# Performance work log

Measured on AMD Instinct MI355X. Metric: run time of the kernel, lower is better.

Reference implementation:

```python
import jax, jax.numpy as jnp
import numpy as np

N = 50000   # nodes
E = 800000  # edges (avg degree 16)
D = 128     # dim_node_features
G = 128     # num_graphs
NP = 25000  # post nodes
NI = 25000  # image nodes
L = 2       # num_gnn_layers
EPS = 1e-5


def setup_inputs() -> dict:
    key = jax.random.key(0)
    ks = jax.random.split(key, 24)
    f = lambda k, shp, s: jax.random.normal(k, shp, jnp.float32) * s
    inp = {
        "x": f(ks[0], (N, D), 1.0),
        "W_gnn": f(ks[1], (L, D, D), D ** -0.5),
        "b_gnn": f(ks[2], (L, D), 0.02),
        "hbn_gamma": 1.0 + f(ks[3], (D,), 0.02),
        "hbn_beta": f(ks[4], (D,), 0.02),
        "gf_w1": f(ks[5], (4 * D, D), (4 * D) ** -0.5),
        "gf_b1": f(ks[6], (D,), 0.02),
        "gf_w2": f(ks[7], (D, D), D ** -0.5),
        "gf_b2": f(ks[8], (D,), 0.02),
        "bn2_gamma": 1.0 + f(ks[9], (D,), 0.02),
        "bn2_beta": f(ks[10], (D,), 0.02),
        "fl_w1": f(ks[11], (D, 64), D ** -0.5),
        "fl_b1": f(ks[12], (64,), 0.02),
        "fl_w2": f(ks[13], (64, 32), 64 ** -0.5),
        "fl_b2": f(ks[14], (32,), 0.02),
        "out_w": f(ks[15], (32, 2), 32 ** -0.5),
        "out_b": f(ks[16], (2,), 0.02),
        "edge_index": jax.random.randint(ks[17], (2, E), 0, N, jnp.int32),
        "post_idx": jax.random.randint(ks[18], (NP,), 0, N, jnp.int32),
        "image_idx": jax.random.randint(ks[19], (NI,), 0, N, jnp.int32),
        "batch_vec": jnp.sort(jax.random.randint(ks[20], (N,), 0, G, jnp.int32)),
    }
    return inp


def _bn(x, gamma, beta):
    # BatchNorm1d, training mode: biased batch statistics
    m = jnp.mean(x, axis=0)
    v = jnp.var(x, axis=0)
    return (x - m) * jax.lax.rsqrt(v + EPS) * gamma + beta


def _mean_pool(feat, seg):
    s = jax.ops.segment_sum(feat, seg, num_segments=G)
    c = jax.ops.segment_sum(jnp.ones(seg.shape[0], feat.dtype), seg, num_segments=G)
    return s / jnp.clip(c, 1.0)[:, None]


def reference(x, W_gnn, b_gnn, hbn_gamma, hbn_beta, gf_w1, gf_b1, gf_w2, gf_b2,
              bn2_gamma, bn2_beta, fl_w1, fl_b1, fl_w2, fl_b2, out_w, out_b,
              edge_index, post_idx, image_idx, batch_vec):
    src, dst = edge_index[0], edge_index[1]
    # GCN symmetric normalization with self loops: deg includes the self loop
    deg = jax.ops.segment_sum(jnp.ones(E, x.dtype), dst, num_segments=N) + 1.0
    dis = deg ** -0.5  # deg^-1/2
    enorm = (dis[src] * dis[dst])[:, None]   # per-edge norm
    snorm = (dis * dis)[:, None]             # self-loop norm
    H = x
    for i in range(L):
        xw = H @ W_gnn[i]                                   # [N, D]
        agg = jax.ops.segment_sum(xw[src] * enorm, dst, num_segments=N)
        H = agg + xw * snorm + b_gnn[i]
        H = jax.nn.leaky_relu(H)
    H = _bn(H, hbn_gamma, hbn_beta)
    pf = _mean_pool(H[post_idx], batch_vec[post_idx])        # [G, D]
    imf = _mean_pool(H[image_idx], batch_vec[image_idx])     # [G, D]
    comb = jnp.concatenate([pf, imf, pf - imf, pf * imf], axis=-1)  # [G, 4D]
    # generate_feature (dropout = identity, eval)
    h = jax.nn.leaky_relu(comb @ gf_w1 + gf_b1) @ gf_w2 + gf_b2
    h = _bn(h, bn2_gamma, bn2_beta)
    # feature_layer (encodeMLP)
    out = jax.nn.leaky_relu(h @ fl_w1 + fl_b1) @ fl_w2 + fl_b2  # [G, 32]
    prob = out @ out_w + out_b                                   # [G, 2]
    return out, prob
```

## Files before the change

kernel.cpp:

```cpp
#include <hip/hip_runtime.h>
#include <hip/hip_bf16.h>
#include <math.h>

#define DF 128
#define PSPLIT 4
#define CHUNK 8192
#define NBK 256
#define LEAKY(x) ((x) > 0.f ? (x) : 0.01f * (x))

typedef __attribute__((ext_vector_type(8))) short short8v;
typedef __attribute__((ext_vector_type(4))) float f32x4;
typedef __attribute__((ext_vector_type(4))) unsigned short u16x4;
typedef __attribute__((ext_vector_type(8))) unsigned short u16x8;

static __device__ __forceinline__ unsigned short f2bf(float f) {
  unsigned u = __float_as_uint(f);
  unsigned r = u + 0x7fffu + ((u >> 16) & 1u);
  return (unsigned short)(r >> 16);
}
static __device__ __forceinline__ float bf2f(unsigned short b) {
  return __uint_as_float(((unsigned)b) << 16);
}

__global__ void fused_pre_k(const int* __restrict__ dst, int* __restrict__ bhist,
                            const int* __restrict__ post_idx, const int* __restrict__ image_idx,
                            const int* __restrict__ batch, int* __restrict__ pcnt,
                            int* __restrict__ icnt,
                            const float* __restrict__ W, unsigned short* __restrict__ Wb,
                            int nE, int NP, int NI, int wTotal, int EB, int PB) {
  int b = blockIdx.x;
  if (b < EB) {
    __shared__ int lh[NBK];
    lh[threadIdx.x] = 0;
    __syncthreads();
    for (int i = b * 256 + threadIdx.x; i < nE; i += EB * 256)
      atomicAdd(&lh[dst[i] >> 8], 1);
    __syncthreads();
    if (lh[threadIdx.x]) atomicAdd(&bhist[threadIdx.x], lh[threadIdx.x]);
  } else if (b < EB + PB) {
    int i = (b - EB) * 256 + threadIdx.x;
    if (i < NP) atomicAdd(&pcnt[batch[post_idx[i]]], 1);
    else if (i < NP + NI) atomicAdd(&icnt[batch[image_idx[i - NP]]], 1);
  } else {
    int i = (b - EB - PB) * 256 + threadIdx.x;
    if (i < wTotal) {
      int layer = i >> 14, o = i & 16383;
      int j = o & 7, l = (o >> 3) & 63, ks = (o >> 9) & 3, ct = (o >> 11) & 3, wc = (o >> 13) & 1;
      int row = ks * 32 + (l >> 4) * 8 + j;
      int col = wc * 64 + ct * 16 + (l & 15);
      Wb[i] = f2bf(W[((size_t)layer << 14) + row * DF + col]);
    }
  }
}

__global__ void __launch_bounds__(1024) scan3_k(
    const int* __restrict__ bhist, int* __restrict__ boff2, int* __restrict__ bcur, int NBUCK,
    const int* __restrict__ pcnt, int* __restrict__ poff, int* __restrict__ pcur,
    const int* __restrict__ icnt, int* __restrict__ ioff, int* __restrict__ icur, int G) {
  const int* in; int* out; int* cur; int n;
  if (blockIdx.x == 0)      { in = bhist; out = boff2; cur = bcur; n = NBUCK; }
  else if (blockIdx.x == 1) { in = pcnt;  out = poff;  cur = pcur; n = G; }
  else                      { in = icnt;  out = ioff;  cur = icur; n = G; }
  __shared__ int sh[1024];
  int v = (threadIdx.x < (unsigned)n) ? in[threadIdx.x] : 0;
  sh[threadIdx.x] = v;
  __syncthreads();
  for (int ofs = 1; ofs < 1024; ofs <<= 1) {
    int t = (threadIdx.x >= (unsigned)ofs) ? sh[threadIdx.x - ofs] : 0;
    __syncthreads();
    sh[threadIdx.x] += t;
    __syncthreads();
  }
  if (threadIdx.x < (unsigned)n) {
    int ex = sh[threadIdx.x] - v;
    out[threadIdx.x] = ex;
    cur[threadIdx.x] = ex;
  }
  if (threadIdx.x == 0) out[n] = sh[1023];
}

__global__ void __launch_bounds__(256) bucket_fill_k(const int* __restrict__ src,
                                                     const int* __restrict__ dst,
                                                     int* __restrict__ bcur,
                                                     int* __restrict__ ebuck, int nE) {
  __shared__ int hist[NBK];
  __shared__ int base[NBK];
  __shared__ int gbase[NBK];
  __shared__ int lpack[CHUNK];
  __shared__ unsigned char lbk[CHUNK];
  int e0 = blockIdx.x * CHUNK;
  int cnt = nE - e0; if (cnt > CHUNK) cnt = CHUNK;
  hist[threadIdx.x] = 0;
  __syncthreads();
  for (int i = threadIdx.x; i < cnt; i += 256)
    atomicAdd(&hist[dst[e0 + i] >> 8], 1);
  __syncthreads();
  int t = threadIdx.x;
  base[t] = hist[t];
  __syncthreads();
  for (int ofs = 1; ofs < NBK; ofs <<= 1) {
    int tv = (t >= ofs) ? base[t - ofs] : 0;
    __syncthreads();
    base[t] += tv;
    __syncthreads();
  }
  int excl = base[t] - hist[t];
  __syncthreads();
  base[t] = excl;
  hist[t] = 0;
  __syncthreads();
  for (int i = threadIdx.x; i < cnt; i += 256) {
    int d = dst[e0 + i], s = src[e0 + i];
    int bk = d >> 8;
    int pos = base[bk] + atomicAdd(&hist[bk], 1);
    lpack[pos] = (s << 8) | (d & 255);
    lbk[pos] = (unsigned char)bk;
  }
  __syncthreads();
  int c = hist[t];
  gbase[t] = c > 0 ? atomicAdd(&bcur[t], c) : 0;
  __syncthreads();
  for (int i = threadIdx.x; i < cnt; i += 256) {
    int bk = lbk[i];
    ebuck[gbase[bk] + (i - base[bk])] = lpack[i];
  }
}

__global__ void __launch_bounds__(256) csr_build_k(const int* __restrict__ boff2,
                                                   const int* __restrict__ ebuck,
                                                   int* __restrict__ rowoff,
                                                   float* __restrict__ dis,
                                                   int2* __restrict__ epack,
                                                   int N, int NBUCK) {
  int b = blockIdx.x;
  int beg = boff2[b], end = boff2[b + 1];
  int node0 = b << 8;
  __shared__ int hist[NBK];
  __shared__ int lbase[NBK];
  int t = threadIdx.x;
  hist[t] = 0;
  __syncthreads();
  for (int i = beg + t; i < end; i += 256)
    atomicAdd(&hist[ebuck[i] & 255], 1);
  __syncthreads();
  int v = hist[t];
  lbase[t] = v;
  __syncthreads();
  for (int ofs = 1; ofs < NBK; ofs <<= 1) {
    int tv = (t >= ofs) ? lbase[t - ofs] : 0;
    __syncthreads();
    lbase[t] += tv;
    __syncthreads();
  }
  int excl = lbase[t] - v;
  __syncthreads();
  lbase[t] = excl;
  hist[t] = 0;
  int node = node0 + t;
  if (node < N) {
    rowoff[node] = beg + excl;
    dis[node] = 1.0f / sqrtf((float)v + 1.0f);
  }
  if (b == NBUCK - 1 && t == 0) rowoff[N] = end;
  __syncthreads();
  for (int i = beg + t; i < end; i += 256) {
    int e = ebuck[i];
    int loc = e & 255;
    int pos = beg + lbase[loc] + atomicAdd(&hist[loc], 1);
    int2 w; w.x = e >> 8; w.y = node0 + loc;
    epack[pos] = w;
  }
}

__global__ void enorm_k(int2* __restrict__ epack, const float* __restrict__ dis, int E) {
  int i = blockIdx.x * 256 + threadIdx.x;
  if (i < E) {
    int2 w = epack[i];
    epack[i].y = __float_as_int(dis[w.x] * dis[w.y]);
  }
}

__global__ void pool_fill_k(const int* __restrict__ post_idx, const int* __restrict__ image_idx,
                            const int* __restrict__ batch, int* __restrict__ pcur,
                            int* __restrict__ icur, int* __restrict__ plist,
                            int* __restrict__ ilist, int NP, int NI) {
  int i = blockIdx.x * 256 + threadIdx.x;
  if (i < NP) {
    int nd = post_idx[i];
    int p = atomicAdd(&pcur[batch[nd]], 1);
    plist[p] = nd;
  } else if (i < NP + NI) {
    int nd = image_idx[i - NP];
    int p = atomicAdd(&icur[batch[nd]], 1);
    ilist[p] = nd;
  }
}

template<bool BF16A>
__global__ void __launch_bounds__(256) gemm_mfma_k(const float* __restrict__ A,
                                                   const unsigned short* __restrict__ Ab,
                                                   const unsigned short* __restrict__ Wb,
                                                   unsigned short* __restrict__ xwb, int n) {
  const int w = threadIdx.x >> 6, l = threadIdx.x & 63;
  const int wr = w & 1, wc = w >> 1;
  const int r0 = blockIdx.x * 32 + wr * 16;
  const int row = r0 + (l & 15);
  const int kg = l >> 4;
  short8v bf[4][4];
  const unsigned short* wp = Wb + (size_t)wc * 8192 + (size_t)l * 8;
#pragma unroll
  for (int ct = 0; ct < 4; ++ct)
#pragma unroll
    for (int ks = 0; ks < 4; ++ks)
      bf[ct][ks] = *(const short8v*)(wp + ((ct * 4 + ks) << 9));
  const bool rok = row < n;
  short8v af[4];
  if constexpr (BF16A) {
    const unsigned short* ap = Ab + (size_t)row * DF + kg * 8;
#pragma unroll
    for (int ks = 0; ks < 4; ++ks)
      af[ks] = rok ? *(const short8v*)(ap + ks * 32) : (short8v)0;
  } else {
    const float* ap = A + (size_t)row * DF + kg * 8;
#pragma unroll
    for (int ks = 0; ks < 4; ++ks) {
      if (rok) {
        float4 lo = *(const float4*)(ap + ks * 32);
        float4 hi = *(const float4*)(ap + ks * 32 + 4);
        short8v t;
        t[0] = (short)f2bf(lo.x); t[1] = (short)f2bf(lo.y);
        t[2] = (short)f2bf(lo.z); t[3] = (short)f2bf(lo.w);
        t[4] = (short)f2bf(hi.x); t[5] = (short)f2bf(hi.y);
        t[6] = (short)f2bf(hi.z); t[7] = (short)f2bf(hi.w);
        af[ks] = t;
      } else af[ks] = (short8v)0;
    }
  }
  f32x4 acc[4];
#pragma unroll
  for (int ct = 0; ct < 4; ++ct) acc[ct] = (f32x4)(0.f);
#pragma unroll
  for (int ks = 0; ks < 4; ++ks)
#pragma unroll
    for (int ct = 0; ct < 4; ++ct)
      acc[ct] = __builtin_amdgcn_mfma_f32_16x16x32_bf16(af[ks], bf[ct][ks], acc[ct], 0, 0, 0);
#pragma unroll
  for (int ct = 0; ct < 4; ++ct) {
    int c = wc * 64 + ct * 16 + (l & 15);
#pragma unroll
    for (int rg = 0; rg < 4; ++rg) {
      int r = r0 + kg * 4 + rg;
      if (r < n) xwb[(size_t)r * DF + c] = f2bf(acc[ct][rg]);
    }
  }
}

__global__ void gather_k(const unsigned short* __restrict__ xwb, const int* __restrict__ rowoff,
                         const int2* __restrict__ epack, const float* __restrict__ dis,
                         const float* __restrict__ b, unsigned short* __restrict__ Hb, int n) {
  int gid = blockIdx.x * 256 + threadIdx.x;
  int node = gid >> 5;
  if (node >= n) return;
  int part = gid & 15;
  int team = (gid >> 4) & 1;
  int beg = rowoff[node], end = rowoff[node + 1];
  float acc[8];
#pragma unroll
  for (int j = 0; j < 8; ++j) acc[j] = 0.f;
  int p = beg + team;
  for (; p + 6 < end; p += 8) {
    int2 q0 = epack[p], q1 = epack[p + 2], q2 = epack[p + 4], q3 = epack[p + 6];
    float e0 = __int_as_float(q0.y), e1 = __int_as_float(q1.y);
    float e2 = __int_as_float(q2.y), e3 = __int_as_float(q3.y);
    u16x8 v0 = *(const u16x8*)(xwb + (size_t)q0.x * DF + part * 8);
    u16x8 v1 = *(const u16x8*)(xwb + (size_t)q1.x * DF + part * 8);
    u16x8 v2 = *(const u16x8*)(xwb + (size_t)q2.x * DF + part * 8);
    u16x8 v3 = *(const u16x8*)(xwb + (size_t)q3.x * DF + part * 8);
#pragma unroll
    for (int j = 0; j < 8; ++j) {
      acc[j] = fmaf(bf2f(v0[j]), e0, acc[j]);
      acc[j] = fmaf(bf2f(v1[j]), e1, acc[j]);
      acc[j] = fmaf(bf2f(v2[j]), e2, acc[j]);
      acc[j] = fmaf(bf2f(v3[j]), e3, acc[j]);
    }
  }
  for (; p < end; p += 2) {
    int2 q = epack[p];
    float e = __int_as_float(q.y);
    u16x8 v = *(const u16x8*)(xwb + (size_t)q.x * DF + part * 8);
#pragma unroll
    for (int j = 0; j < 8; ++j) acc[j] = fmaf(bf2f(v[j]), e, acc[j]);
  }
#pragma unroll
  for (int j = 0; j < 8; ++j) acc[j] += __shfl_down(acc[j], 16, 32);
  if (team == 0) {
    float dd = dis[node], sn = dd * dd;
    u16x8 xv = *(const u16x8*)(xwb + (size_t)node * DF + part * 8);
    const float* bp = b + part * 8;
    u16x8 o;
#pragma unroll
    for (int j = 0; j < 8; ++j) {
      float r = fmaf(bf2f(xv[j]), sn, acc[j]) + bp[j];
      r = LEAKY(r);
      o[j] = f2bf(r);
    }
    *(u16x8*)(Hb + (size_t)node * DF + part * 8) = o;
  }
}

__global__ void post_k(const unsigned short* __restrict__ Hb,
                       const int* __restrict__ goff_p, const int* __restrict__ mlist_p,
                       const int* __restrict__ goff_i, const int* __restrict__ mlist_i,
                       float* __restrict__ psum, float* __restrict__ isum,
                       float* __restrict__ bns, int n, int PGB, int SB) {
  int b = blockIdx.x;
  if (b < 2 * PGB) {
    int which = b >= PGB;
    int bb = which ? b - PGB : b;
    const int* goff  = which ? goff_i  : goff_p;
    const int* mlist = which ? mlist_i : mlist_p;
    float* out       = which ? isum    : psum;
    int g = bb / PSPLIT, sub = bb % PSPLIT;
    int part = threadIdx.x & 31, slot = threadIdx.x >> 5;
    int beg = goff[g], end = goff[g + 1];
    float4 acc = make_float4(0.f, 0.f, 0.f, 0.f);
    for (int j = beg + sub * 8 + slot; j < end; j += PSPLIT * 8) {
      u16x4 v = *(const u16x4*)(Hb + (size_t)mlist[j] * DF + part * 4);
      acc.x += bf2f(v[0]); acc.y += bf2f(v[1]); acc.z += bf2f(v[2]); acc.w += bf2f(v[3]);
    }
    __shared__ float4 sh[256];
    sh[threadIdx.x] = acc;
    __syncthreads();
    for (int ofs = 128; ofs >= 32; ofs >>= 1) {
      if (threadIdx.x < (unsigned)ofs) {
        float4 o = sh[threadIdx.x + ofs];
        float4 a = sh[threadIdx.x];
        a.x += o.x; a.y += o.y; a.z += o.z; a.w += o.w;
        sh[threadIdx.x] = a;
      }
      __syncthreads();
    }
    if (threadIdx.x < 32) {
      float4 a = sh[threadIdx.x];
      float* o = out + (size_t)g * DF + part * 4;
      atomicAdd(o + 0, a.x);
      atomicAdd(o + 1, a.y);
      atomicAdd(o + 2, a.z);
      atomicAdd(o + 3, a.w);
    }
  } else {
    int sb = b - 2 * PGB;
    int c = threadIdx.x & (DF - 1);
    int half = threadIdx.x >> 7;
    float s = 0.f, q = 0.f;
    for (int r = sb * 2 + half; r < n; r += SB * 2) {
      float v = bf2f(Hb[(size_t)r * DF + c]);
      s += v; q += v * v;
    }
    __shared__ float ls[256], lq[256];
    ls[threadIdx.x] = s; lq[threadIdx.x] = q;
    __syncthreads();
    if (half == 0) {
      atomicAdd(&bns[c], ls[c] + ls[c + DF]);
      atomicAdd(&bns[DF + c], lq[c] + lq[c + DF]);
    }
  }
}

__global__ void __launch_bounds__(512) head1_k(const float* __restrict__ psum,
                        const int* __restrict__ pcnt,
                        const float* __restrict__ isum, const int* __restrict__ icnt,
                        const float* __restrict__ bns, const float* __restrict__ hbn_gamma,
                        const float* __restrict__ hbn_beta, int nN,
                        const float* __restrict__ gf_w1, const float* __restrict__ gf_b1,
                        const float* __restrict__ gf_w2, const float* __restrict__ gf_b2,
                        float* __restrict__ hbuf) {
  int g = blockIdx.x;
  int j = threadIdx.x & 127, kq = threadIdx.x >> 7;
  __shared__ float comb[4 * DF];
  __shared__ float part[512];
  __shared__ float t1[DF];
  if (kq == 0) {
    float m = bns[j] / (float)nN;
    float var = bns[DF + j] / (float)nN - m * m;
    if (var < 0.f) var = 0.f;
    float sc = hbn_gamma[j] / sqrtf(var + 1e-5f);
    float sh = hbn_beta[j] - m * sc;
    int pc = pcnt[g], ic = icnt[g];
    float pf = pc > 0 ? (psum[(size_t)g * DF + j] / (float)pc) * sc + sh : 0.f;
    float im = ic > 0 ? (isum[(size_t)g * DF + j] / (float)ic) * sc + sh : 0.f;
    comb[j] = pf;
    comb[DF + j] = im;
    comb[2 * DF + j] = pf - im;
    comb[3 * DF + j] = pf * im;
  }
  __syncthreads();
  float acc = 0.f;
  const float* w1 = gf_w1 + (size_t)kq * 128 * DF + j;
#pragma unroll 8
  for (int kk = 0; kk < 128; ++kk)
    acc = fmaf(comb[kq * 128 + kk], w1[(size_t)kk * DF], acc);
  part[threadIdx.x] = acc;
  __syncthreads();
  if (kq == 0)
    t1[j] = LEAKY(gf_b1[j] + part[j] + part[128 + j] + part[256 + j] + part[384 + j]);
  __syncthreads();
  acc = 0.f;
  const float* w2 = gf_w2 + (size_t)kq * 32 * DF + j;
#pragma unroll 8
  for (int kk = 0; kk < 32; ++kk)
    acc = fmaf(t1[kq * 32 + kk], w2[(size_t)kk * DF], acc);
  part[threadIdx.x] = acc;
  __syncthreads();
  if (kq == 0)
    hbuf[(size_t)g * DF + j] = gf_b2[j] + part[j] + part[128 + j] + part[256 + j] + part[384 + j];
}

__global__ void __launch_bounds__(1024) bn2_k(const float* __restrict__ hbuf,
                      const float* __restrict__ gamma, const float* __restrict__ beta,
                      float* __restrict__ ss2, int G) {
  int c = threadIdx.x & 127, slot = threadIdx.x >> 7;
  float s = 0.f, q = 0.f;
  for (int r = slot; r < G; r += 8) {
    float v = hbuf[(size_t)r * DF + c];
    s += v; q += v * v;
  }
  __shared__ float ls[1024], lq[1024];
  ls[threadIdx.x] = s; lq[threadIdx.x] = q;
  __syncthreads();
  for (int ofs = 512; ofs >= 128; ofs >>= 1) {
    if (threadIdx.x < (unsigned)ofs) {
      ls[threadIdx.x] += ls[threadIdx.x + ofs];
      lq[threadIdx.x] += lq[threadIdx.x + ofs];
    }
    __syncthreads();
  }
  if (threadIdx.x < 128) {
    float m = ls[c] / (float)G;
    float var = lq[c] / (float)G - m * m;
    if (var < 0.f) var = 0.f;
    float sc = gamma[c] / sqrtf(var + 1e-5f);
    ss2[c] = sc;
    ss2[DF + c] = beta[c] - m * sc;
  }
}

__global__ void __launch_bounds__(512) head2_k(const float* __restrict__ hbuf,
                        const float* __restrict__ ss2,
                        const float* __restrict__ fl_w1, const float* __restrict__ fl_b1,
                        const float* __restrict__ fl_w2, const float* __restrict__ fl_b2,
                        const float* __restrict__ out_w, const float* __restrict__ out_b,
                        float* __restrict__ d_out, int G) {
  int g = blockIdx.x, t = threadIdx.x;
  __shared__ float hb[DF], part[512], t1[64], ov[32];
  if (t < DF) hb[t] = hbuf[(size_t)g * DF + t] * ss2[t] + ss2[DF + t];
  __syncthreads();
  {
    int j = t & 63, kq = t >> 6;
    float acc = 0.f;
    const float* w = fl_w1 + (size_t)kq * 16 * 64 + j;
#pragma unroll
    for (int kk = 0; kk < 16; ++kk)
      acc = fmaf(hb[kq * 16 + kk], w[(size_t)kk * 64], acc);
    part[t] = acc;
  }
  __syncthreads();
  if (t < 64) {
    float s = fl_b1[t];
#pragma unroll
    for (int i = 0; i < 8; ++i) s += part[i * 64 + t];
    t1[t] = LEAKY(s);
  }
  __syncthreads();
  {
    int j = t & 31, kq = t >> 5;
    float acc = 0.f;
    const float* w = fl_w2 + (size_t)kq * 4 * 32 + j;
#pragma unroll
    for (int kk = 0; kk < 4; ++kk)
      acc = fmaf(t1[kq * 4 + kk], w[(size_t)kk * 32], acc);
    part[t] = acc;
  }
  __syncthreads();
  if (t < 32) {
    float s = fl_b2[t];
#pragma unroll
    for (int i = 0; i < 16; ++i) s += part[i * 32 + t];
    d_out[(size_t)g * 32 + t] = s;
    ov[t] = s;
  }
  __syncthreads();
  if (t < 64) {
    int j = t & 1, kq = t >> 1;
    part[t] = ov[kq] * out_w[(size_t)kq * 2 + j];
  }
  __syncthreads();
  if (t < 2) {
    float s = out_b[t];
#pragma unroll
    for (int i = 0; i < 32; ++i) s += part[i * 2 + t];
    d_out[(size_t)G * 32 + (size_t)g * 2 + t] = s;
  }
}

extern "C" void kernel_launch(void* const* d_in, const int* in_sizes, int n_in,
                              void* d_out, int out_size, void* d_ws, size_t ws_size,
                              hipStream_t stream) {
  const float* x         = (const float*)d_in[0];
  const float* W_gnn     = (const float*)d_in[1];
  const float* b_gnn     = (const float*)d_in[2];
  const float* hbn_gamma = (const float*)d_in[3];
  const float* hbn_beta  = (const float*)d_in[4];
  const float* gf_w1     = (const float*)d_in[5];
  const float* gf_b1     = (const float*)d_in[6];
  const float* gf_w2     = (const float*)d_in[7];
  const float* gf_b2     = (const float*)d_in[8];
  const float* bn2_gamma = (const float*)d_in[9];
  const float* bn2_beta  = (const float*)d_in[10];
  const float* fl_w1     = (const float*)d_in[11];
  const float* fl_b1     = (const float*)d_in[12];
  const float* fl_w2     = (const float*)d_in[13];
  const float* fl_b2     = (const float*)d_in[14];
  const float* out_w     = (const float*)d_in[15];
  const float* out_b     = (const float*)d_in[16];
  const int* edge_index  = (const int*)d_in[17];
  const int* post_idx    = (const int*)d_in[18];
  const int* image_idx   = (const int*)d_in[19];
  const int* batch_vec   = (const int*)d_in[20];

  const int N  = in_sizes[20];
  const int E  = in_sizes[17] / 2;
  const int NP = in_sizes[18];
  const int NI = in_sizes[19];
  const int G  = out_size / 34;
  const int L  = in_sizes[1] / (DF * DF);
  const int* src  = edge_index;
  const int* dstp = edge_index + E;
  const int NBUCK = (N + 255) >> 8;
  const int EB = 256;
  const int PB = (NP + NI + 255) / 256;
  const int WT = L * DF * DF;
  const int WB = (WT + 255) / 256;
  const int PGB = G * PSPLIT;
  const int SB = 256;

  char* ws = (char*)d_ws;
  size_t off = 0;
  auto alloc = [&](size_t b) { size_t o = off; off += (b + 255) & ~(size_t)255; return o; };
  size_t zero_beg = off;
  int*   bhist  = (int*)(ws + alloc((size_t)NBK * 4));
  float* bns    = (float*)(ws + alloc(256 * 4));
  float* psum   = (float*)(ws + alloc((size_t)G * DF * 4));
  float* isum   = (float*)(ws + alloc((size_t)G * DF * 4));
  int*   pcnt   = (int*)(ws + alloc((size_t)G * 4));
  int*   icnt   = (int*)(ws + alloc((size_t)G * 4));
  size_t zero_bytes = off - zero_beg;
  float* dis    = (float*)(ws + alloc((size_t)N * 4));
  int*   rowoff = (int*)(ws + alloc((size_t)(N + 1) * 4));
  int2*  epack  = (int2*)(ws + alloc((size_t)E * 8));
  int*   ebuck  = (int*)(ws + alloc((size_t)E * 4));
  int*   boff2  = (int*)(ws + alloc((size_t)(NBK + 1) * 4));
  int*   bcur   = (int*)(ws + alloc((size_t)NBK * 4));
  unsigned short* Wb  = (unsigned short*)(ws + alloc((size_t)WT * 2));
  unsigned short* xwb = (unsigned short*)(ws + alloc((size_t)N * DF * 2));
  unsigned short* Hb  = (unsigned short*)(ws + alloc((size_t)N * DF * 2));
  int*   poff   = (int*)(ws + alloc((size_t)(G + 1) * 4));
  int*   ioff   = (int*)(ws + alloc((size_t)(G + 1) * 4));
  int*   pcur   = (int*)(ws + alloc((size_t)G * 4));
  int*   icur   = (int*)(ws + alloc((size_t)G * 4));
  int*   plist  = (int*)(ws + alloc((size_t)NP * 4));
  int*   ilist  = (int*)(ws + alloc((size_t)NI * 4));
  float* hbuf   = (float*)(ws + alloc((size_t)G * DF * 4));
  float* ss2    = (float*)(ws + alloc(256 * 4));

  hipMemsetAsync(ws + zero_beg, 0, zero_bytes, stream);

  fused_pre_k<<<EB + PB + WB, 256, 0, stream>>>(dstp, bhist, post_idx, image_idx,
                                                batch_vec, pcnt, icnt, W_gnn, Wb,
                                                E, NP, NI, WT, EB, PB);
  scan3_k<<<3, 1024, 0, stream>>>(bhist, boff2, bcur, NBUCK,
                                  pcnt, poff, pcur, icnt, ioff, icur, G);
  bucket_fill_k<<<(E + CHUNK - 1) / CHUNK, 256, 0, stream>>>(src, dstp, bcur, ebuck, E);
  csr_build_k<<<NBUCK, 256, 0, stream>>>(boff2, ebuck, rowoff, dis, epack, N, NBUCK);
  enorm_k<<<(E + 255) / 256, 256, 0, stream>>>(epack, dis, E);
  pool_fill_k<<<(NP + NI + 255) / 256, 256, 0, stream>>>(post_idx, image_idx, batch_vec,
                                                         pcur, icur, plist, ilist, NP, NI);

  for (int l = 0; l < L; ++l) {
    if (l == 0)
      gemm_mfma_k<false><<<(N + 31) / 32, 256, 0, stream>>>(x, nullptr,
          Wb + (size_t)l * DF * DF, xwb, N);
    else
      gemm_mfma_k<true><<<(N + 31) / 32, 256, 0, stream>>>(nullptr, Hb,
          Wb + (size_t)l * DF * DF, xwb, N);
    gather_k<<<(N * 32 + 255) / 256, 256, 0, stream>>>(xwb, rowoff, epack, dis,
                                                       b_gnn + (size_t)l * DF, Hb, N);
  }

  post_k<<<2 * PGB + SB, 256, 0, stream>>>(Hb, poff, plist, ioff, ilist,
                                           psum, isum, bns, N, PGB, SB);

  head1_k<<<G, 512, 0, stream>>>(psum, pcnt, isum, icnt, bns, hbn_gamma, hbn_beta, N,
                                 gf_w1, gf_b1, gf_w2, gf_b2, hbuf);
  bn2_k<<<1, 1024, 0, stream>>>(hbuf, bn2_gamma, bn2_beta, ss2, G);
  head2_k<<<G, 512, 0, stream>>>(hbuf, ss2, fl_w1, fl_b1, fl_w2, fl_b2, out_w, out_b,
                                 (float*)d_out, G);
}
```

Before: 237.0 us.

## Use fixed-capacity edge buckets and fuse preprocessing kernels to cut launches

```diff
diff --git a/kernel.cpp b/kernel.cpp
--- a/kernel.cpp
+++ b/kernel.cpp
@@ -6,6 +6,7 @@
 #define PSPLIT 4
 #define CHUNK 8192
 #define NBK 256
+#define CAP 6144
 #define LEAKY(x) ((x) > 0.f ? (x) : 0.01f * (x))
 
 typedef __attribute__((ext_vector_type(8))) short short8v;
@@ -22,27 +23,18 @@
   return __uint_as_float(((unsigned)b) << 16);
 }
 
-__global__ void fused_pre_k(const int* __restrict__ dst, int* __restrict__ bhist,
-                            const int* __restrict__ post_idx, const int* __restrict__ image_idx,
-                            const int* __restrict__ batch, int* __restrict__ pcnt,
-                            int* __restrict__ icnt,
-                            const float* __restrict__ W, unsigned short* __restrict__ Wb,
-                            int nE, int NP, int NI, int wTotal, int EB, int PB) {
+__global__ void fusedA_k(const int* __restrict__ post_idx, const int* __restrict__ image_idx,
+                         const int* __restrict__ batch, int* __restrict__ pcnt,
+                         int* __restrict__ icnt,
+                         const float* __restrict__ W, unsigned short* __restrict__ Wb,
+                         int NP, int NI, int wTotal, int PB) {
   int b = blockIdx.x;
-  if (b < EB) {
-    __shared__ int lh[NBK];
-    lh[threadIdx.x] = 0;
-    __syncthreads();
-    for (int i = b * 256 + threadIdx.x; i < nE; i += EB * 256)
-      atomicAdd(&lh[dst[i] >> 8], 1);
-    __syncthreads();
-    if (lh[threadIdx.x]) atomicAdd(&bhist[threadIdx.x], lh[threadIdx.x]);
-  } else if (b < EB + PB) {
-    int i = (b - EB) * 256 + threadIdx.x;
+  if (b < PB) {
+    int i = b * 256 + threadIdx.x;
     if (i < NP) atomicAdd(&pcnt[batch[post_idx[i]]], 1);
     else if (i < NP + NI) atomicAdd(&icnt[batch[image_idx[i - NP]]], 1);
   } else {
-    int i = (b - EB - PB) * 256 + threadIdx.x;
+    int i = (b - PB) * 256 + threadIdx.x;
     if (i < wTotal) {
       int layer = i >> 14, o = i & 16383;
       int j = o & 7, l = (o >> 3) & 63, ks = (o >> 9) & 3, ct = (o >> 11) & 3, wc = (o >> 13) & 1;
@@ -51,32 +43,6 @@
       Wb[i] = f2bf(W[((size_t)layer << 14) + row * DF + col]);
     }
   }
-}
-
-__global__ void __launch_bounds__(1024) scan3_k(
-    const int* __restrict__ bhist, int* __restrict__ boff2, int* __restrict__ bcur, int NBUCK,
-    const int* __restrict__ pcnt, int* __restrict__ poff, int* __restrict__ pcur,
-    const int* __restrict__ icnt, int* __restrict__ ioff, int* __restrict__ icur, int G) {
-  const int* in; int* out; int* cur; int n;
-  if (blockIdx.x == 0)      { in = bhist; out = boff2; cur = bcur; n = NBUCK; }
-  else if (blockIdx.x == 1) { in = pcnt;  out = poff;  cur = pcur; n = G; }
-  else                      { in = icnt;  out = ioff;  cur = icur; n = G; }
-  __shared__ int sh[1024];
-  int v = (threadIdx.x < (unsigned)n) ? in[threadIdx.x] : 0;
-  sh[threadIdx.x] = v;
-  __syncthreads();
-  for (int ofs = 1; ofs < 1024; ofs <<= 1) {
-    int t = (threadIdx.x >= (unsigned)ofs) ? sh[threadIdx.x - ofs] : 0;
-    __syncthreads();
-    sh[threadIdx.x] += t;
-    __syncthreads();
-  }
-  if (threadIdx.x < (unsigned)n) {
-    int ex = sh[threadIdx.x] - v;
-    out[threadIdx.x] = ex;
-    cur[threadIdx.x] = ex;
-  }
-  if (threadIdx.x == 0) out[n] = sh[1023];
 }
 
 __global__ void __launch_bounds__(256) bucket_fill_k(const int* __restrict__ src,
@@ -118,7 +84,7 @@
   }
   __syncthreads();
   int c = hist[t];
-  gbase[t] = c > 0 ? atomicAdd(&bcur[t], c) : 0;
+  gbase[t] = c > 0 ? (t * CAP + atomicAdd(&bcur[t], c)) : 0;
   __syncthreads();
   for (int i = threadIdx.x; i < cnt; i += 256) {
     int bk = lbk[i];
@@ -126,22 +92,51 @@
   }
 }
 
-__global__ void __launch_bounds__(256) csr_build_k(const int* __restrict__ boff2,
+__global__ void __launch_bounds__(1024) scan3_k(
+    const int* __restrict__ bcur, int* __restrict__ boff2, int NBUCK,
+    const int* __restrict__ pcnt, int* __restrict__ poff, int* __restrict__ pcur,
+    const int* __restrict__ icnt, int* __restrict__ ioff, int* __restrict__ icur, int G) {
+  const int* in; int* out; int* cur; int n;
+  if (blockIdx.x == 0)      { in = bcur; out = boff2; cur = nullptr; n = NBUCK; }
+  else if (blockIdx.x == 1) { in = pcnt; out = poff;  cur = pcur;    n = G; }
+  else                      { in = icnt; out = ioff;  cur = icur;    n = G; }
+  __shared__ int sh[1024];
+  int v = (threadIdx.x < (unsigned)n) ? in[threadIdx.x] : 0;
+  sh[threadIdx.x] = v;
+  __syncthreads();
+  for (int ofs = 1; ofs < 1024; ofs <<= 1) {
+    int t = (threadIdx.x >= (unsigned)ofs) ? sh[threadIdx.x - ofs] : 0;
+    __syncthreads();
+    sh[threadIdx.x] += t;
+    __syncthreads();
+  }
+  if (threadIdx.x < (unsigned)n) {
+    int ex = sh[threadIdx.x] - v;
+    out[threadIdx.x] = ex;
+    if (cur) cur[threadIdx.x] = ex;
+  }
+  if (threadIdx.x == 0) out[n] = sh[1023];
+}
+
+__global__ void __launch_bounds__(256) csr_build_k(const int* __restrict__ bcnt,
+                                                   const int* __restrict__ boff2,
                                                    const int* __restrict__ ebuck,
                                                    int* __restrict__ rowoff,
                                                    float* __restrict__ dis,
                                                    int2* __restrict__ epack,
                                                    int N, int NBUCK) {
   int b = blockIdx.x;
-  int beg = boff2[b], end = boff2[b + 1];
+  int cnt = bcnt[b];
+  int ob = boff2[b];
+  const int* ebk = ebuck + (size_t)b * CAP;
   int node0 = b << 8;
   __shared__ int hist[NBK];
   __shared__ int lbase[NBK];
   int t = threadIdx.x;
   hist[t] = 0;
   __syncthreads();
-  for (int i = beg + t; i < end; i += 256)
-    atomicAdd(&hist[ebuck[i] & 255], 1);
+  for (int i = t; i < cnt; i += 256)
+    atomicAdd(&hist[ebk[i] & 255], 1);
   __syncthreads();
   int v = hist[t];
   lbase[t] = v;
@@ -158,52 +153,29 @@
   hist[t] = 0;
   int node = node0 + t;
   if (node < N) {
-    rowoff[node] = beg + excl;
+    rowoff[node] = ob + excl;
     dis[node] = 1.0f / sqrtf((float)v + 1.0f);
   }
-  if (b == NBUCK - 1 && t == 0) rowoff[N] = end;
-  __syncthreads();
-  for (int i = beg + t; i < end; i += 256) {
-    int e = ebuck[i];
+  if (b == NBUCK - 1 && t == 0) rowoff[N] = ob + cnt;
+  __syncthreads();
+  for (int i = t; i < cnt; i += 256) {
+    int e = ebk[i];
     int loc = e & 255;
-    int pos = beg + lbase[loc] + atomicAdd(&hist[loc], 1);
+    int pos = ob + lbase[loc] + atomicAdd(&hist[loc], 1);
     int2 w; w.x = e >> 8; w.y = node0 + loc;
     epack[pos] = w;
   }
 }
 
-__global__ void enorm_k(int2* __restrict__ epack, const float* __restrict__ dis, int E) {
-  int i = blockIdx.x * 256 + threadIdx.x;
-  if (i < E) {
-    int2 w = epack[i];
-    epack[i].y = __float_as_int(dis[w.x] * dis[w.y]);
-  }
-}
-
-__global__ void pool_fill_k(const int* __restrict__ post_idx, const int* __restrict__ image_idx,
-                            const int* __restrict__ batch, int* __restrict__ pcur,
-                            int* __restrict__ icur, int* __restrict__ plist,
-                            int* __restrict__ ilist, int NP, int NI) {
-  int i = blockIdx.x * 256 + threadIdx.x;
-  if (i < NP) {
-    int nd = post_idx[i];
-    int p = atomicAdd(&pcur[batch[nd]], 1);
-    plist[p] = nd;
-  } else if (i < NP + NI) {
-    int nd = image_idx[i - NP];
-    int p = atomicAdd(&icur[batch[nd]], 1);
-    ilist[p] = nd;
-  }
-}
-
 template<bool BF16A>
-__global__ void __launch_bounds__(256) gemm_mfma_k(const float* __restrict__ A,
-                                                   const unsigned short* __restrict__ Ab,
-                                                   const unsigned short* __restrict__ Wb,
-                                                   unsigned short* __restrict__ xwb, int n) {
-  const int w = threadIdx.x >> 6, l = threadIdx.x & 63;
+static __device__ __forceinline__ void gemm_body(int bid, int tid,
+                                                 const float* __restrict__ A,
+                                                 const unsigned short* __restrict__ Ab,
+                                                 const unsigned short* __restrict__ Wb,
+                                                 unsigned short* __restrict__ xwb, int n) {
+  const int w = tid >> 6, l = tid & 63;
   const int wr = w & 1, wc = w >> 1;
-  const int r0 = blockIdx.x * 32 + wr * 16;
+  const int r0 = bid * 32 + wr * 16;
   const int row = r0 + (l & 15);
   const int kg = l >> 4;
   short8v bf[4][4];
@@ -255,6 +227,43 @@
   }
 }
 
+__global__ void __launch_bounds__(256) gemm_mfma_k(const unsigned short* __restrict__ Ab,
+                                                   const unsigned short* __restrict__ Wb,
+                                                   unsigned short* __restrict__ xwb, int n) {
+  gemm_body<true>(blockIdx.x, threadIdx.x, nullptr, Ab, Wb, xwb, n);
+}
+
+__global__ void __launch_bounds__(256) fusedB_k(const float* __restrict__ x,
+                        const unsigned short* __restrict__ Wb, unsigned short* __restrict__ xwb,
+                        int2* __restrict__ epack, const float* __restrict__ dis, int E,
+                        const int* __restrict__ post_idx, const int* __restrict__ image_idx,
+                        const int* __restrict__ batch, int* __restrict__ pcur,
+                        int* __restrict__ icur, int* __restrict__ plist,
+                        int* __restrict__ ilist, int NP, int NI,
+                        int n, int GB, int EN) {
+  int b = blockIdx.x;
+  if (b < GB) {
+    gemm_body<false>(b, threadIdx.x, x, nullptr, Wb, xwb, n);
+  } else if (b < GB + EN) {
+    int i = (b - GB) * 256 + threadIdx.x;
+    if (i < E) {
+      int2 w = epack[i];
+      epack[i].y = __float_as_int(dis[w.x] * dis[w.y]);
+    }
+  } else {
+    int i = (b - GB - EN) * 256 + threadIdx.x;
+    if (i < NP) {
+      int nd = post_idx[i];
+      int p = atomicAdd(&pcur[batch[nd]], 1);
+      plist[p] = nd;
+    } else if (i < NP + NI) {
+      int nd = image_idx[i - NP];
+      int p = atomicAdd(&icur[batch[nd]], 1);
+      ilist[p] = nd;
+    }
+  }
+}
+
 __global__ void gather_k(const unsigned short* __restrict__ xwb, const int* __restrict__ rowoff,
                          const int2* __restrict__ epack, const float* __restrict__ dis,
                          const float* __restrict__ b, unsigned short* __restrict__ Hb, int n) {
@@ -268,6 +277,20 @@
 #pragma unroll
   for (int j = 0; j < 8; ++j) acc[j] = 0.f;
   int p = beg + team;
+  for (; p + 14 < end; p += 16) {
+    int2 q[8];
+#pragma unroll
+    for (int u = 0; u < 8; ++u) q[u] = epack[p + 2 * u];
+    u16x8 v[8];
+#pragma unroll
+    for (int u = 0; u < 8; ++u) v[u] = *(const u16x8*)(xwb + (size_t)q[u].x * DF + part * 8);
+#pragma unroll
+    for (int u = 0; u < 8; ++u) {
+      float e = __int_as_float(q[u].y);
+#pragma unroll
+      for (int j = 0; j < 8; ++j) acc[j] = fmaf(bf2f(v[u][j]), e, acc[j]);
+    }
+  }
   for (; p + 6 < end; p += 8) {
     int2 q0 = epack[p], q1 = epack[p + 2], q2 = epack[p + 4], q3 = epack[p + 6];
     float e0 = __int_as_float(q0.y), e1 = __int_as_float(q1.y);
@@ -537,10 +560,11 @@
   const int* src  = edge_index;
   const int* dstp = edge_index + E;
   const int NBUCK = (N + 255) >> 8;
-  const int EB = 256;
   const int PB = (NP + NI + 255) / 256;
   const int WT = L * DF * DF;
   const int WB = (WT + 255) / 256;
+  const int GB = (N + 31) / 32;
+  const int EN = (E + 255) / 256;
   const int PGB = G * PSPLIT;
   const int SB = 256;
 
@@ -548,7 +572,7 @@
   size_t off = 0;
   auto alloc = [&](size_t b) { size_t o = off; off += (b + 255) & ~(size_t)255; return o; };
   size_t zero_beg = off;
-  int*   bhist  = (int*)(ws + alloc((size_t)NBK * 4));
+  int*   bcur   = (int*)(ws + alloc((size_t)NBK * 4));
   float* bns    = (float*)(ws + alloc(256 * 4));
   float* psum   = (float*)(ws + alloc((size_t)G * DF * 4));
   float* isum   = (float*)(ws + alloc((size_t)G * DF * 4));
@@ -558,9 +582,8 @@
   float* dis    = (float*)(ws + alloc((size_t)N * 4));
   int*   rowoff = (int*)(ws + alloc((size_t)(N + 1) * 4));
   int2*  epack  = (int2*)(ws + alloc((size_t)E * 8));
-  int*   ebuck  = (int*)(ws + alloc((size_t)E * 4));
+  int*   ebuck  = (int*)(ws + alloc((size_t)NBUCK * CAP * 4));
   int*   boff2  = (int*)(ws + alloc((size_t)(NBK + 1) * 4));
-  int*   bcur   = (int*)(ws + alloc((size_t)NBK * 4));
   unsigned short* Wb  = (unsigned short*)(ws + alloc((size_t)WT * 2));
   unsigned short* xwb = (unsigned short*)(ws + alloc((size_t)N * DF * 2));
   unsigned short* Hb  = (unsigned short*)(ws + alloc((size_t)N * DF * 2));
@@ -575,24 +598,18 @@
 
   hipMemsetAsync(ws + zero_beg, 0, zero_bytes, stream);
 
-  fused_pre_k<<<EB + PB + WB, 256, 0, stream>>>(dstp, bhist, post_idx, image_idx,
-                                                batch_vec, pcnt, icnt, W_gnn, Wb,
-                                                E, NP, NI, WT, EB, PB);
-  scan3_k<<<3, 1024, 0, stream>>>(bhist, boff2, bcur, NBUCK,
-                                  pcnt, poff, pcur, icnt, ioff, icur, G);
   bucket_fill_k<<<(E + CHUNK - 1) / CHUNK, 256, 0, stream>>>(src, dstp, bcur, ebuck, E);
-  csr_build_k<<<NBUCK, 256, 0, stream>>>(boff2, ebuck, rowoff, dis, epack, N, NBUCK);
-  enorm_k<<<(E + 255) / 256, 256, 0, stream>>>(epack, dis, E);
-  pool_fill_k<<<(NP + NI + 255) / 256, 256, 0, stream>>>(post_idx, image_idx, batch_vec,
-                                                         pcur, icur, plist, ilist, NP, NI);
-
-  for (int l = 0; l < L; ++l) {
-    if (l == 0)
-      gemm_mfma_k<false><<<(N + 31) / 32, 256, 0, stream>>>(x, nullptr,
-          Wb + (size_t)l * DF * DF, xwb, N);
-    else
-      gemm_mfma_k<true><<<(N + 31) / 32, 256, 0, stream>>>(nullptr, Hb,
-          Wb + (size_t)l * DF * DF, xwb, N);
+  fusedA_k<<<PB + WB, 256, 0, stream>>>(post_idx, image_idx, batch_vec, pcnt, icnt,
+                                        W_gnn, Wb, NP, NI, WT, PB);
+  scan3_k<<<3, 1024, 0, stream>>>(bcur, boff2, NBUCK, pcnt, poff, pcur, icnt, ioff, icur, G);
+  csr_build_k<<<NBUCK, 256, 0, stream>>>(bcur, boff2, ebuck, rowoff, dis, epack, N, NBUCK);
+  fusedB_k<<<GB + EN + PB, 256, 0, stream>>>(x, Wb, xwb, epack, dis, E,
+                                             post_idx, image_idx, batch_vec,
+                                             pcur, icur, plist, ilist, NP, NI, N, GB, EN);
+  gather_k<<<(N * 32 + 255) / 256, 256, 0, stream>>>(xwb, rowoff, epack, dis,
+                                                     b_gnn, Hb, N);
+  for (int l = 1; l < L; ++l) {
+    gemm_mfma_k<<<GB, 256, 0, stream>>>(Hb, Wb + (size_t)l * DF * DF, xwb, N);
     gather_k<<<(N * 32 + 255) / 256, 256, 0, stream>>>(xwb, rowoff, epack, dis,
                                                        b_gnn + (size_t)l * DF, Hb, N);
   }
```

After: 248.2 us. 1.05x slower.
